# Kernel optimization log

Measured on AMD Instinct MI355X. Metric: run time of the kernel, lower is better.

Reference implementation:

```python
import jax, jax.numpy as jnp
import numpy as np

NUM_NODES = 500000
NUM_SAMPLED = 10
DIM = 256
N = 65536


def setup_inputs() -> dict:
    key = jax.random.key(0)
    k1, k2, k3, k4 = jax.random.split(key, 4)
    u = jax.random.randint(k1, (N,), 0, NUM_NODES, dtype=jnp.int64 if jax.config.jax_enable_x64 else jnp.int32)
    v = jax.random.randint(k2, (N,), 0, NUM_NODES, dtype=u.dtype)
    # degree=None -> uniform weights; multinomial with replacement == uniform randint
    negs = jax.random.randint(k3, (N, NUM_SAMPLED), 0, NUM_NODES, dtype=u.dtype)
    embs = jax.random.normal(k4, (NUM_NODES, DIM), dtype=jnp.float32)
    return {"u": u, "v": v, "negs": negs, "embs": embs}


def reference(u, v, negs, embs):
    eu = embs[u]                      # [n, d]
    ev = embs[v]                      # [n, d]
    # log(sigmoid(<e_u, e_v>)) per positive pair
    log_target = jax.nn.log_sigmoid(jnp.sum(eu * ev, axis=1))          # [n]
    noise = -embs[negs]               # [n, k, d]
    scores = jnp.einsum("nkd,nd->nk", noise, eu)                       # [n, k]
    sum_log_sampled = jnp.sum(jax.nn.log_sigmoid(scores), axis=1)      # [n]
    loss = log_target + sum_log_sampled
    n = u.shape[0]
    return -jnp.sum(loss) / n
```

## Files before the change

kernel.cpp:

```cpp
#include <hip/hip_runtime.h>


#define DIM 256
#define NUM_SAMPLED 10

__device__ __forceinline__ float wave_reduce_sum(float x) {
#pragma unroll
    for (int off = 32; off > 0; off >>= 1)
        x += __shfl_xor(x, off, 64);
    return x;
}

__device__ __forceinline__ float log_sigmoid(float x) {
    return fminf(x, 0.0f) - log1pf(expf(-fabsf(x)));
}

__global__ void zero_out_kernel(float* out) { *out = 0.0f; }

__global__ __launch_bounds__(256) void neg_loss_kernel(
    const int* __restrict__ u,
    const int* __restrict__ v,
    const int* __restrict__ negs,
    const float* __restrict__ embs,
    float* __restrict__ out,
    int n)
{
    const int lane = threadIdx.x & 63;
    const int wave_in_block = threadIdx.x >> 6;
    const int gwave = (blockIdx.x * blockDim.x + threadIdx.x) >> 6;
    const int waves_total = (gridDim.x * blockDim.x) >> 6;

    float acc = 0.0f;

    for (int i = gwave; i < n; i += waves_total) {
        const int ui = u[i];
        const int vi = v[i];

        const float4 eu = *reinterpret_cast<const float4*>(embs + (size_t)ui * DIM + lane * 4);
        const float4 ev = *reinterpret_cast<const float4*>(embs + (size_t)vi * DIM + lane * 4);

        float pos = eu.x * ev.x + eu.y * ev.y + eu.z * ev.z + eu.w * ev.w;

        float s[NUM_SAMPLED];
#pragma unroll
        for (int k = 0; k < NUM_SAMPLED; ++k) {
            const int nk = negs[i * NUM_SAMPLED + k];
            const float4 en = *reinterpret_cast<const float4*>(embs + (size_t)nk * DIM + lane * 4);
            s[k] = -(eu.x * en.x + eu.y * en.y + eu.z * en.z + eu.w * en.w);
        }

        float loss = log_sigmoid(wave_reduce_sum(pos));
#pragma unroll
        for (int k = 0; k < NUM_SAMPLED; ++k) {
            loss += log_sigmoid(wave_reduce_sum(s[k]));
        }
        acc += loss;
    }

    __shared__ float wave_acc[4];
    if (lane == 0) wave_acc[wave_in_block] = acc;
    __syncthreads();
    if (threadIdx.x == 0) {
        float b = wave_acc[0] + wave_acc[1] + wave_acc[2] + wave_acc[3];
        atomicAdd(out, b * (-1.0f / n));
    }
}

extern "C" void kernel_launch(void* const* d_in, const int* in_sizes, int n_in,
                              void* d_out, int out_size, void* d_ws, size_t ws_size,
                              hipStream_t stream) {
    const int*   u    = (const int*)d_in[0];
    const int*   v    = (const int*)d_in[1];
    const int*   negs = (const int*)d_in[2];
    const float* embs = (const float*)d_in[3];
    float* out = (float*)d_out;

    const int n = in_sizes[0];

    zero_out_kernel<<<1, 1, 0, stream>>>(out);

    const int blocks = 2048;
    neg_loss_kernel<<<blocks, 256, 0, stream>>>(u, v, negs, embs, out, n);
}
```

Baseline: 721.1 us.

## Map each sample to a 16-lane group with cooperative index loads

Replaces the one-wave-per-sample grid-stride loop with 16-lane groups, each handling one sample, and launches one block per 16 samples. The u/v/neg indices are loaded once per group by separate lanes and shared through shuffles, not reloaded as a broadcast by every lane. Dot-product reductions now need only four shuffle stages across 16 lanes, batched over all 11 scores. This cuts shuffle and reduction overhead and raises memory-level parallelism, at the cost of many more blocks and one atomic per block.

```diff
diff --git a/kernel.cpp b/kernel.cpp
--- a/kernel.cpp
+++ b/kernel.cpp
@@ -3,13 +3,6 @@
 
 #define DIM 256
 #define NUM_SAMPLED 10
-
-__device__ __forceinline__ float wave_reduce_sum(float x) {
-#pragma unroll
-    for (int off = 32; off > 0; off >>= 1)
-        x += __shfl_xor(x, off, 64);
-    return x;
-}
 
 __device__ __forceinline__ float log_sigmoid(float x) {
     return fminf(x, 0.0f) - log1pf(expf(-fabsf(x)));
@@ -25,43 +18,73 @@
     float* __restrict__ out,
     int n)
 {
-    const int lane = threadIdx.x & 63;
-    const int wave_in_block = threadIdx.x >> 6;
-    const int gwave = (blockIdx.x * blockDim.x + threadIdx.x) >> 6;
-    const int waves_total = (gridDim.x * blockDim.x) >> 6;
+    const int lane16 = threadIdx.x & 15;
+    const int group  = threadIdx.x >> 4;
+    const int i      = blockIdx.x * 16 + group;
+    const int wbase  = threadIdx.x & 48;
 
-    float acc = 0.0f;
-
-    for (int i = gwave; i < n; i += waves_total) {
-        const int ui = u[i];
-        const int vi = v[i];
-
-        const float4 eu = *reinterpret_cast<const float4*>(embs + (size_t)ui * DIM + lane * 4);
-        const float4 ev = *reinterpret_cast<const float4*>(embs + (size_t)vi * DIM + lane * 4);
-
-        float pos = eu.x * ev.x + eu.y * ev.y + eu.z * ev.z + eu.w * ev.w;
-
-        float s[NUM_SAMPLED];
-#pragma unroll
-        for (int k = 0; k < NUM_SAMPLED; ++k) {
-            const int nk = negs[i * NUM_SAMPLED + k];
-            const float4 en = *reinterpret_cast<const float4*>(embs + (size_t)nk * DIM + lane * 4);
-            s[k] = -(eu.x * en.x + eu.y * en.y + eu.z * en.z + eu.w * en.w);
-        }
-
-        float loss = log_sigmoid(wave_reduce_sum(pos));
-#pragma unroll
-        for (int k = 0; k < NUM_SAMPLED; ++k) {
-            loss += log_sigmoid(wave_reduce_sum(s[k]));
-        }
-        acc += loss;
+    int idx = 0;
+    if (i < n) {
+        if (lane16 < NUM_SAMPLED)        idx = negs[(size_t)i * NUM_SAMPLED + lane16];
+        else if (lane16 == NUM_SAMPLED)  idx = u[i];
+        else if (lane16 == 11)           idx = v[i];
     }
 
-    __shared__ float wave_acc[4];
-    if (lane == 0) wave_acc[wave_in_block] = acc;
+    const int iu = __shfl(idx, wbase + 10, 64);
+    const int iv = __shfl(idx, wbase + 11, 64);
+    int ik[NUM_SAMPLED];
+#pragma unroll
+    for (int k = 0; k < NUM_SAMPLED; ++k) ik[k] = __shfl(idx, wbase + k, 64);
+
+    const float* pu = embs + (size_t)iu * DIM + lane16 * 4;
+    const float* pv = embs + (size_t)iv * DIM + lane16 * 4;
+
+    float4 eu[4];
+#pragma unroll
+    for (int c = 0; c < 4; ++c) eu[c] = *reinterpret_cast<const float4*>(pu + c * 64);
+
+    float s[NUM_SAMPLED + 1];
+
+    {
+        float p = 0.0f;
+#pragma unroll
+        for (int c = 0; c < 4; ++c) {
+            const float4 ev = *reinterpret_cast<const float4*>(pv + c * 64);
+            p += eu[c].x * ev.x + eu[c].y * ev.y + eu[c].z * ev.z + eu[c].w * ev.w;
+        }
+        s[0] = p;
+    }
+
+#pragma unroll
+    for (int k = 0; k < NUM_SAMPLED; ++k) {
+        const float* pn = embs + (size_t)ik[k] * DIM + lane16 * 4;
+        float d = 0.0f;
+#pragma unroll
+        for (int c = 0; c < 4; ++c) {
+            const float4 en = *reinterpret_cast<const float4*>(pn + c * 64);
+            d += eu[c].x * en.x + eu[c].y * en.y + eu[c].z * en.z + eu[c].w * en.w;
+        }
+        s[k + 1] = -d;
+    }
+
+#pragma unroll
+    for (int off = 1; off < 16; off <<= 1) {
+#pragma unroll
+        for (int j = 0; j < NUM_SAMPLED + 1; ++j)
+            s[j] += __shfl_xor(s[j], off, 64);
+    }
+
+    float loss = 0.0f;
+#pragma unroll
+    for (int j = 0; j < NUM_SAMPLED + 1; ++j) loss += log_sigmoid(s[j]);
+
+    __shared__ float g_acc[16];
+    if (lane16 == 0) g_acc[group] = (i < n) ? loss : 0.0f;
     __syncthreads();
     if (threadIdx.x == 0) {
-        float b = wave_acc[0] + wave_acc[1] + wave_acc[2] + wave_acc[3];
+        float b = 0.0f;
+#pragma unroll
+        for (int g = 0; g < 16; ++g) b += g_acc[g];
         atomicAdd(out, b * (-1.0f / n));
     }
 }
@@ -79,6 +102,6 @@
 
     zero_out_kernel<<<1, 1, 0, stream>>>(out);
 
-    const int blocks = 2048;
+    const int blocks = (n + 15) / 16;
     neg_loss_kernel<<<blocks, 256, 0, stream>>>(u, v, negs, embs, out, n);
 }
```

New measurement: 673.0 us. -6.7%, faster.
